# Optimization experiments

Hardware: AMD Instinct MI355X
Metric: run time of the kernel (lower is better)

The kernel has to match this reference:

```python
import jax, jax.numpy as jnp
import numpy as np

DIM = 512
D = 256
SCALE = D ** (-0.5)


def setup_inputs() -> dict:
    key = jax.random.key(0)
    ks = jax.random.split(key, 7)
    B, N, K = 16, 4096, 32
    g = 0.1 * (6.0 / (DIM + D)) ** 0.5  # xavier_uniform with gain=0.1
    return {
        "E_patches": jax.random.normal(ks[0], (B, N, DIM), jnp.float32),
        "T_b5": jax.random.normal(ks[1], (B, K, DIM), jnp.float32),
        "P_batch": jax.random.uniform(ks[2], (B, N), jnp.float32),
        "Wq": jax.random.uniform(ks[3], (D, DIM), jnp.float32, -g, g),
        "Wk": jax.random.uniform(ks[4], (D, DIM), jnp.float32, -g, g),
        "Wv": jax.random.uniform(ks[5], (D, DIM), jnp.float32, -g, g),
        "Wo": jax.random.uniform(ks[6], (DIM, D), jnp.float32, -g, g),
    }


def reference(E_patches, T_b5, P_batch, Wq, Wk, Wv, Wo):
    # Projections (torch Linear: x @ W.T)
    Q = jnp.einsum('bkm,dm->bkd', T_b5, Wq)       # [B,K,D]
    Kp = jnp.einsum('bnm,dm->bnd', E_patches, Wk)  # [B,N,D]
    V = jnp.einsum('bnm,dm->bnd', E_patches, Wv)   # [B,N,D]
    scores = jnp.einsum('bkd,bnd->bkn', Q, Kp) * SCALE
    logP = jnp.log(jnp.clip(P_batch, 0.1, 0.9))    # [B,N]
    scores = scores + logP[:, None, :]             # additive log-prior bias
    A = jax.nn.softmax(scores, axis=-1)            # [B,K,N]
    F_agg = jnp.einsum('bkn,bnd->bkd', A, V)
    F_agg = jnp.einsum('bkd,md->bkm', F_agg, Wo)   # [B,K,DIM]
    F_agg = F_agg / (jnp.linalg.norm(F_agg, axis=-1, keepdims=True) + 1e-8)
    return (F_agg, A)
```

## Files before the change

### kernel.cpp

```cpp
#include <hip/hip_runtime.h>

typedef __bf16 bf16x8 __attribute__((ext_vector_type(8)));
typedef __bf16 bf16x4 __attribute__((ext_vector_type(4)));
typedef float  f32x4  __attribute__((ext_vector_type(4)));

__device__ __forceinline__ void cp16(void* lds, const void* g) {
  __builtin_amdgcn_global_load_lds(
      (const __attribute__((address_space(1))) unsigned int*)g,
      (__attribute__((address_space(3))) unsigned int*)lds, 16, 0, 0);
}

#define VMCNT0  asm volatile("s_waitcnt vmcnt(0)" ::: "memory")
#define LGKM0   asm volatile("s_waitcnt lgkmcnt(0)" ::: "memory")
#define BARRAW  __builtin_amdgcn_s_barrier
#define MFMA    __builtin_amdgcn_mfma_f32_16x16x32_bf16


__global__ __launch_bounds__(256) void cvt_small(const float* __restrict__ Wq,
                                                 const float* __restrict__ Wk,
                                                 const float* __restrict__ Wv,
                                                 const float* __restrict__ Wo,
                                                 const float* __restrict__ T,
                                                 __bf16* __restrict__ Wqb,
                                                 __bf16* __restrict__ Tbf,
                                                 __bf16* __restrict__ WkT,
                                                 float* __restrict__ WvT,
                                                 float* __restrict__ WoT) {
  const int idx = blockIdx.x * 256 + threadIdx.x;
  if (idx < 32768) {
    const int o = idx * 4;
    f32x4 v = *(const f32x4*)(Wq + o);
    bf16x4 b;
    b[0] = (__bf16)v[0]; b[1] = (__bf16)v[1];
    b[2] = (__bf16)v[2]; b[3] = (__bf16)v[3];
    *(bf16x4*)(Wqb + o) = b;
  } else if (idx < 98304) {
    const int o = (idx - 32768) * 4;
    f32x4 v = *(const f32x4*)(T + o);
    bf16x4 b;
    b[0] = (__bf16)v[0]; b[1] = (__bf16)v[1];
    b[2] = (__bf16)v[2]; b[3] = (__bf16)v[3];
    *(bf16x4*)(Tbf + o) = b;
  } else if (idx < 106496) {
    const int t2 = idx - 98304;
    const int d0 = (t2 >> 7) * 4, m0 = (t2 & 127) * 4;
    f32x4 r0 = *(const f32x4*)(Wk + (size_t)(d0 + 0) * 512 + m0);
    f32x4 r1 = *(const f32x4*)(Wk + (size_t)(d0 + 1) * 512 + m0);
    f32x4 r2 = *(const f32x4*)(Wk + (size_t)(d0 + 2) * 512 + m0);
    f32x4 r3 = *(const f32x4*)(Wk + (size_t)(d0 + 3) * 512 + m0);
#pragma unroll
    for (int j = 0; j < 4; ++j) {
      bf16x4 o;
      o[0] = (__bf16)r0[j]; o[1] = (__bf16)r1[j];
      o[2] = (__bf16)r2[j]; o[3] = (__bf16)r3[j];
      *(bf16x4*)(WkT + (size_t)(m0 + j) * 256 + d0) = o;
    }
  } else if (idx < 114688) {
    const int t2 = idx - 106496;
    const int d0 = (t2 >> 7) * 4, m0 = (t2 & 127) * 4;
    f32x4 r0 = *(const f32x4*)(Wv + (size_t)(d0 + 0) * 512 + m0);
    f32x4 r1 = *(const f32x4*)(Wv + (size_t)(d0 + 1) * 512 + m0);
    f32x4 r2 = *(const f32x4*)(Wv + (size_t)(d0 + 2) * 512 + m0);
    f32x4 r3 = *(const f32x4*)(Wv + (size_t)(d0 + 3) * 512 + m0);
#pragma unroll
    for (int j = 0; j < 4; ++j) {
      f32x4 o;
      o[0] = r0[j]; o[1] = r1[j]; o[2] = r2[j]; o[3] = r3[j];
      *(f32x4*)(WvT + (size_t)(m0 + j) * 256 + d0) = o;
    }
  } else {
    const int t2 = idx - 114688;
    const int m0 = (t2 >> 6) * 4, d0 = (t2 & 63) * 4;
    f32x4 r0 = *(const f32x4*)(Wo + (size_t)(m0 + 0) * 256 + d0);
    f32x4 r1 = *(const f32x4*)(Wo + (size_t)(m0 + 1) * 256 + d0);
    f32x4 r2 = *(const f32x4*)(Wo + (size_t)(m0 + 2) * 256 + d0);
    f32x4 r3 = *(const f32x4*)(Wo + (size_t)(m0 + 3) * 256 + d0);
#pragma unroll
    for (int j = 0; j < 4; ++j) {
      f32x4 o;
      o[0] = r0[j]; o[1] = r1[j]; o[2] = r2[j]; o[3] = r3[j];
      *(f32x4*)(WoT + (size_t)(d0 + j) * 512 + m0) = o;
    }
  }
}

__global__ __launch_bounds__(256) void qproj(const __bf16* __restrict__ Wqb,
                                             const __bf16* __restrict__ Tbf,
                                             __bf16* __restrict__ Qw) {
  __shared__ __align__(16) __bf16 At[4096];
  __shared__ __align__(16) __bf16 Bt[4096];
  const int tid = threadIdx.x, lane = tid & 63;
  const int q = lane >> 4, ln = lane & 15;
  const int w = tid >> 6, wm = w >> 1, wn = w & 1;
  const int t = blockIdx.x;
  const int nbase = (t & 3) * 128;
  const int mbase = (t >> 2) * 128;
  f32x4 acc[4][4] = {};
  for (int kt = 0; kt < 16; ++kt) {
    const int k0 = kt * 32;
    __syncthreads();
#pragma unroll
    for (int s = 0; s < 2; ++s) {
      const int cbase = (tid & 192) + s * 256;
      const int cc = cbase + lane;
      const int row = cc >> 2, kc = (cc & 3) * 8;
      cp16(&At[cbase * 8], Wqb + (size_t)(mbase + row) * 512 + k0 + kc);
      cp16(&Bt[cbase * 8], Tbf + (size_t)(nbase + row) * 512 + k0 + kc);
    }
    __syncthreads();
    bf16x8 af[4], bfr[4];
#pragma unroll
    for (int f = 0; f < 4; ++f) {
      af[f]  = *(const bf16x8*)&At[(wm * 64 + f * 16 + ln) * 32 + q * 8];
      bfr[f] = *(const bf16x8*)&Bt[(wn * 64 + f * 16 + ln) * 32 + q * 8];
    }
#pragma unroll
    for (int fm = 0; fm < 4; ++fm)
#pragma unroll
      for (int fn = 0; fn < 4; ++fn)
        acc[fm][fn] = MFMA(af[fm], bfr[fn], acc[fm][fn], 0, 0, 0);
  }
#pragma unroll
  for (int fm = 0; fm < 4; ++fm)
#pragma unroll
    for (int fn = 0; fn < 4; ++fn) {
      const int m = mbase + wm * 64 + fm * 16 + q * 4;
      const int n = nbase + wn * 64 + fn * 16 + ln;
      f32x4 v = acc[fm][fn];
      bf16x4 o;
      o[0] = (__bf16)v[0]; o[1] = (__bf16)v[1];
      o[2] = (__bf16)v[2]; o[3] = (__bf16)v[3];
      *(bf16x4*)&Qw[(size_t)n * 256 + m] = o;
    }
}

__global__ __launch_bounds__(256) void qwk(const __bf16* __restrict__ WkT,
                                           const __bf16* __restrict__ Qwp,
                                           __bf16* __restrict__ QWkb) {
  __shared__ __align__(16) __bf16 At[4096];
  __shared__ __align__(16) __bf16 Bt[4096];
  const int tid = threadIdx.x, lane = tid & 63;
  const int q = lane >> 4, ln = lane & 15;
  const int w = tid >> 6, wm = w >> 1, wn = w & 1;
  const int t = blockIdx.x;
  const int nbase = (t & 3) * 128;
  const int mbase = (t >> 2) * 128;
  f32x4 acc[4][4] = {};
  for (int kt = 0; kt < 8; ++kt) {
    const int k0 = kt * 32;
    __syncthreads();
#pragma unroll
    for (int s = 0; s < 2; ++s) {
      const int cbase = (tid & 192) + s * 256;
      const int cc = cbase + lane;
      const int row = cc >> 2, kc = (cc & 3) * 8;
      cp16(&At[cbase * 8], WkT + (size_t)(mbase + row) * 256 + k0 + kc);
      cp16(&Bt[cbase * 8], Qwp + (size_t)(nbase + row) * 256 + k0 + kc);
    }
    __syncthreads();
    bf16x8 af[4], bfr[4];
#pragma unroll
    for (int f = 0; f < 4; ++f) {
      af[f]  = *(const bf16x8*)&At[(wm * 64 + f * 16 + ln) * 32 + q * 8];
      bfr[f] = *(const bf16x8*)&Bt[(wn * 64 + f * 16 + ln) * 32 + q * 8];
    }
#pragma unroll
    for (int fm = 0; fm < 4; ++fm)
#pragma unroll
      for (int fn = 0; fn < 4; ++fn)
        acc[fm][fn] = MFMA(af[fm], bfr[fn], acc[fm][fn], 0, 0, 0);
  }
#pragma unroll
  for (int fm = 0; fm < 4; ++fm)
#pragma unroll
    for (int fn = 0; fn < 4; ++fn) {
      const int m = mbase + wm * 64 + fm * 16 + q * 4;
      const int n = nbase + wn * 64 + fn * 16 + ln;
      f32x4 v = acc[fm][fn];
      bf16x4 o;
      o[0] = (__bf16)v[0]; o[1] = (__bf16)v[1];
      o[2] = (__bf16)v[2]; o[3] = (__bf16)v[3];
      *(bf16x4*)&QWkb[(size_t)n * 512 + m] = o;
    }
}

__device__ __forceinline__ void load_e(f32x4 (&ev)[16], const float* Eb,
                                       int s, int rg, int cg0) {
#pragma unroll
  for (int i = 0; i < 4; ++i) {
    const int cg = cg0 + i * 32;
#pragma unroll
    for (int r = 0; r < 4; ++r)
      ev[i * 4 + r] = *(const f32x4*)(Eb + (size_t)(s * 32 + rg * 4 + r) * 512 + cg * 4);
  }
}
__device__ __forceinline__ void cvtwrite_e(const f32x4 (&ev)[16], __bf16* Er,
                                           char* EtT, int rg, int cg0) {
#pragma unroll
  for (int i = 0; i < 4; ++i) {
    const int cg = cg0 + i * 32;
#pragma unroll
    for (int r = 0; r < 4; ++r) {
      bf16x4 rw;
      rw[0] = (__bf16)ev[i*4+r][0]; rw[1] = (__bf16)ev[i*4+r][1];
      rw[2] = (__bf16)ev[i*4+r][2]; rw[3] = (__bf16)ev[i*4+r][3];
      *(bf16x4*)((char*)Er + (size_t)(rg * 4 + r) * 1040 + cg * 8) = rw;
    }
#pragma unroll
    for (int j = 0; j < 4; ++j) {
      bf16x4 tw;
      tw[0] = (__bf16)ev[i*4+0][j]; tw[1] = (__bf16)ev[i*4+1][j];
      tw[2] = (__bf16)ev[i*4+2][j]; tw[3] = (__bf16)ev[i*4+3][j];
      const int m = cg * 4 + j;
      const int u = (rg >> 1) ^ (m & 3);
      *(bf16x4*)(EtT + (size_t)m * 80 + u * 16 + (rg & 1) * 8) = tw;
    }
  }
}
__device__ __forceinline__ void phase1(int s, const bf16x8 (&qf)[16],
                                       const __bf16* Er, __bf16* Plds,
                                       const float* Lp, float* rsum,
                                       int kf, int nf, int q, int ln) {
  f32x4 sacc = {0.f, 0.f, 0.f, 0.f};
#pragma unroll
  for (int kk = 0; kk < 16; ++kk) {
    bf16x8 bb = *(const bf16x8*)((char*)Er + (size_t)(nf * 16 + ln) * 1040 + kk * 64 + q * 16);
    sacc = MFMA(qf[kk], bb, sacc, 0, 0, 0);
  }
  const float lp = Lp[s * 32 + nf * 16 + ln];
  float pv[4];
#pragma unroll
  for (int r = 0; r < 4; ++r) {
    pv[r] = __expf(sacc[r] * 0.0625f + lp);
    *((__bf16*)((char*)Plds + (size_t)(kf * 16 + q * 4 + r) * 80) + nf * 16 + ln) = (__bf16)pv[r];
  }
#pragma unroll
  for (int mm = 1; mm < 16; mm <<= 1)
#pragma unroll
    for (int r = 0; r < 4; ++r) pv[r] += __shfl_xor(pv[r], mm, 64);
  if (ln == 0) {
#pragma unroll
    for (int r = 0; r < 4; ++r) atomicAdd(&rsum[kf * 16 + q * 4 + r], pv[r]);
  }
}
__device__ __forceinline__ void phase2(f32x4 (&facc)[2][8], const __bf16* Plds,
                                       const char* EtT, int w, int q, int ln,
                                       int tid, bf16x4* pr) {
  bf16x8 pa0 = *(const bf16x8*)((char*)Plds + (size_t)(ln) * 80 + q * 16);
  bf16x8 pa1 = *(const bf16x8*)((char*)Plds + (size_t)(16 + ln) * 80 + q * 16);
#pragma unroll
  for (int mf = 0; mf < 8; ++mf) {
    const int m = w * 128 + mf * 16 + ln;
    const int u = q ^ (m & 3);
    bf16x8 vb = *(const bf16x8*)(EtT + (size_t)m * 80 + u * 16);
    facc[0][mf] = MFMA(pa0, vb, facc[0][mf], 0, 0, 0);
    facc[1][mf] = MFMA(pa1, vb, facc[1][mf], 0, 0, 0);
  }
  *pr = *(const bf16x4*)((char*)Plds + (size_t)(tid >> 3) * 80 + (tid & 7) * 8);
}

__global__ __launch_bounds__(256, 2) void fused_main(
    const float* __restrict__ E, const __bf16* __restrict__ QWkb,
    const float* __restrict__ Pb, __bf16* __restrict__ Pws,
    float* __restrict__ Fpart, float* __restrict__ rowsum) {
  __shared__ __align__(16) __bf16 Er[32 * 520];
  __shared__ __align__(16) char  EtT[512 * 80];
  __shared__ __align__(16) __bf16 Plds[32 * 40];
  __shared__ __align__(16) float Lp[128];
  __shared__ float rsum[32];

  const int tid = threadIdx.x;
  const int lane = tid & 63;
  const int q = lane >> 4, ln = lane & 15;
  const int w = tid >> 6;
  const int kf = w >> 1;
  const int nf = w & 1;
  const int b = blockIdx.y, c = blockIdx.x;
  const int rg = tid >> 5;
  const int cg0 = tid & 31;

  const float* Eb = E + ((size_t)b * 4096 + (size_t)c * 128) * 512;

  bf16x8 qf[16];
  {
    const __bf16* qr = QWkb + (size_t)(b * 32 + kf * 16 + ln) * 512 + q * 8;
#pragma unroll
    for (int kk = 0; kk < 16; ++kk) qf[kk] = *(const bf16x8*)(qr + kk * 32);
  }
  if (tid < 128) {
    float p = Pb[b * 4096 + c * 128 + tid];
    Lp[tid] = __logf(fminf(fmaxf(p, 0.1f), 0.9f));
  }
  if (tid < 32) rsum[tid] = 0.f;

  f32x4 ev[16];
  load_e(ev, Eb, 0, rg, cg0);

  f32x4 facc[2][8] = {};
  bf16x4 pr0, pr1, pr2, pr3;

  VMCNT0;
  cvtwrite_e(ev, Er, EtT, rg, cg0);
  load_e(ev, Eb, 1, rg, cg0);
  LGKM0; BARRAW();
  phase1(0, qf, Er, Plds, Lp, rsum, kf, nf, q, ln);
  LGKM0; BARRAW();
  phase2(facc, Plds, EtT, w, q, ln, tid, &pr0);
  BARRAW();
  VMCNT0;
  cvtwrite_e(ev, Er, EtT, rg, cg0);
  load_e(ev, Eb, 2, rg, cg0);
  LGKM0; BARRAW();
  phase1(1, qf, Er, Plds, Lp, rsum, kf, nf, q, ln);
  LGKM0; BARRAW();
  phase2(facc, Plds, EtT, w, q, ln, tid, &pr1);
  BARRAW();
  VMCNT0;
  cvtwrite_e(ev, Er, EtT, rg, cg0);
  load_e(ev, Eb, 3, rg, cg0);
  LGKM0; BARRAW();
  phase1(2, qf, Er, Plds, Lp, rsum, kf, nf, q, ln);
  LGKM0; BARRAW();
  phase2(facc, Plds, EtT, w, q, ln, tid, &pr2);
  BARRAW();
  VMCNT0;
  cvtwrite_e(ev, Er, EtT, rg, cg0);
  LGKM0; BARRAW();
  phase1(3, qf, Er, Plds, Lp, rsum, kf, nf, q, ln);
  LGKM0; BARRAW();
  phase2(facc, Plds, EtT, w, q, ln, tid, &pr3);

  {
    const int prow = tid >> 3, pc = (tid & 7) * 4;
    __bf16* pwr = Pws + (size_t)(b * 32 + prow) * 4096 + c * 128 + pc;
    *(bf16x4*)(pwr)      = pr0;
    *(bf16x4*)(pwr + 32) = pr1;
    *(bf16x4*)(pwr + 64) = pr2;
    *(bf16x4*)(pwr + 96) = pr3;
  }
  float* Fp = Fpart + ((size_t)c * 512 + b * 32) * 512;
#pragma unroll
  for (int kf2 = 0; kf2 < 2; ++kf2)
#pragma unroll
    for (int mf = 0; mf < 8; ++mf)
#pragma unroll
      for (int r = 0; r < 4; ++r)
        Fp[(size_t)(kf2 * 16 + q * 4 + r) * 512 + w * 128 + mf * 16 + ln] = facc[kf2][mf][r];
  if (tid < 32) atomicAdd(&rowsum[b * 32 + tid], rsum[tid]);
}

__global__ __launch_bounds__(256) void norm_p(const __bf16* __restrict__ Pws,
                                              const float* __restrict__ rowsum,
                                              float* __restrict__ Aout) {
  const size_t idx = ((size_t)blockIdx.x * 256 + threadIdx.x) * 4;
  const int row = (int)(idx >> 12);
  const float invs = 1.0f / rowsum[row];
  bf16x4 p = *(const bf16x4*)(Pws + idx);
  f32x4 o;
  o[0] = (float)p[0] * invs; o[1] = (float)p[1] * invs;
  o[2] = (float)p[2] * invs; o[3] = (float)p[3] * invs;
  *(f32x4*)(Aout + idx) = o;
}

__global__ __launch_bounds__(256) void final_kernel(const float* __restrict__ Fpart,
                                                    const float* __restrict__ WvT,
                                                    const float* __restrict__ WoT,
                                                    float* __restrict__ Fout) {
  __shared__ float fl[512];
  __shared__ float agg[256];
  __shared__ float f2b[512];
  __shared__ float redbuf[4];
  const int row = blockIdx.x;
  const int t = threadIdx.x;
  const int lane = t & 63;
  const int w = t >> 6;

  {
    float s0 = 0.f, s1 = 0.f;
#pragma unroll
    for (int cc = 0; cc < 32; ++cc) {
      const float* p = Fpart + (size_t)cc * 262144 + (size_t)row * 512;
      s0 += p[t]; s1 += p[t + 256];
    }
    fl[t] = s0; fl[t + 256] = s1;
  }
  __syncthreads();

  {
    float a0 = 0.f, a1 = 0.f, a2 = 0.f, a3 = 0.f;
    for (int m = 0; m < 512; m += 4) {
      a0 += fl[m]     * WvT[(size_t)(m + 0) * 256 + t];
      a1 += fl[m + 1] * WvT[(size_t)(m + 1) * 256 + t];
      a2 += fl[m + 2] * WvT[(size_t)(m + 2) * 256 + t];
      a3 += fl[m + 3] * WvT[(size_t)(m + 3) * 256 + t];
    }
    agg[t] = (a0 + a1) + (a2 + a3);
  }
  __syncthreads();

  {
    float b0 = 0.f, b1 = 0.f, b2 = 0.f, b3 = 0.f;
    float c0 = 0.f, c1 = 0.f, c2 = 0.f, c3 = 0.f;
    for (int d = 0; d < 256; d += 4) {
      const float g0 = agg[d], g1 = agg[d + 1], g2 = agg[d + 2], g3 = agg[d + 3];
      b0 += g0 * WoT[(size_t)(d + 0) * 512 + t];
      b1 += g1 * WoT[(size_t)(d + 1) * 512 + t];
      b2 += g2 * WoT[(size_t)(d + 2) * 512 + t];
      b3 += g3 * WoT[(size_t)(d + 3) * 512 + t];
      c0 += g0 * WoT[(size_t)(d + 0) * 512 + t + 256];
      c1 += g1 * WoT[(size_t)(d + 1) * 512 + t + 256];
      c2 += g2 * WoT[(size_t)(d + 2) * 512 + t + 256];
      c3 += g3 * WoT[(size_t)(d + 3) * 512 + t + 256];
    }
    f2b[t] = (b0 + b1) + (b2 + b3);
    f2b[t + 256] = (c0 + c1) + (c2 + c3);
  }
  __syncthreads();

  {
    const float x0 = f2b[t], x1 = f2b[t + 256];
    float ps = x0 * x0 + x1 * x1;
#pragma unroll
    for (int mm = 1; mm < 64; mm <<= 1) ps += __shfl_xor(ps, mm, 64);
    if (lane == 0) redbuf[w] = ps;
  }
  __syncthreads();
  {
    const float tot = redbuf[0] + redbuf[1] + redbuf[2] + redbuf[3];
    const float sc = 1.0f / (sqrtf(tot) + 1e-8f);
    Fout[(size_t)row * 512 + t] = f2b[t] * sc;
    Fout[(size_t)row * 512 + t + 256] = f2b[t + 256] * sc;
  }
}

extern "C" void kernel_launch(void* const* d_in, const int* in_sizes, int n_in,
                              void* d_out, int out_size, void* d_ws, size_t ws_size,
                              hipStream_t stream) {
  const float* E  = (const float*)d_in[0];
  const float* T  = (const float*)d_in[1];
  const float* Pb = (const float*)d_in[2];
  const float* Wq = (const float*)d_in[3];
  const float* Wk = (const float*)d_in[4];
  const float* Wv = (const float*)d_in[5];
  const float* Wo = (const float*)d_in[6];

  float* out  = (float*)d_out;
  float* Fout = out;
  float* Aout = out + 262144;

  char* ws = (char*)d_ws;
  float*  Fpart = (float*)ws;
  __bf16* Pws   = (__bf16*)(ws + 33554432);
  __bf16* Tbf   = (__bf16*)(ws + 37748736);
  __bf16* Wqb   = (__bf16*)(ws + 38273024);
  __bf16* WkT   = (__bf16*)(ws + 38535168);
  float*  WvT   = (float*)(ws + 38797312);
  __bf16* Qw    = (__bf16*)(ws + 39321600);
  __bf16* QWkb  = (__bf16*)(ws + 39583744);
  float*  rowsum = (float*)(ws + 40108032);
  float*  WoT   = (float*)(ws + 40110080);

  hipMemsetAsync(rowsum, 0, 2048, stream);

  cvt_small<<<480, 256, 0, stream>>>(Wq, Wk, Wv, Wo, T, Wqb, Tbf, WkT, WvT, WoT);
  qproj<<<8, 256, 0, stream>>>(Wqb, Tbf, Qw);
  qwk<<<16, 256, 0, stream>>>(WkT, Qw, QWkb);
  fused_main<<<dim3(32, 16), 256, 0, stream>>>(E, QWkb, Pb, Pws, Fpart, rowsum);
  norm_p<<<2048, 256, 0, stream>>>(Pws, rowsum, Aout);
  final_kernel<<<512, 256, 0, stream>>>(Fpart, WvT, WoT, Fout);
}
```

Before: 268.2 us.

## Halve per-block N tile, read score operand from global, process two rows per final block

The main fused kernel now handles 64 patches per block instead of 128 and launches twice as many blocks. It drops the row-major bf16 LDS copy of E: phase1 reads E straight from global (cache-resident) and converts it in registers, which frees LDS and allows 3 blocks per CU. The cost is that the Fpart partial buffer doubles in size (64 chunks), so the final kernel sums more partials. To offset that, the final kernel handles two rows per block and reuses the Wv/Wo loads across both rows.

```diff
diff --git a/kernel.cpp b/kernel.cpp
--- a/kernel.cpp
+++ b/kernel.cpp
@@ -194,18 +194,11 @@
       ev[i * 4 + r] = *(const f32x4*)(Eb + (size_t)(s * 32 + rg * 4 + r) * 512 + cg * 4);
   }
 }
-__device__ __forceinline__ void cvtwrite_e(const f32x4 (&ev)[16], __bf16* Er,
-                                           char* EtT, int rg, int cg0) {
+__device__ __forceinline__ void cvtwrite_t(const f32x4 (&ev)[16], char* EtT,
+                                           int rg, int cg0) {
 #pragma unroll
   for (int i = 0; i < 4; ++i) {
     const int cg = cg0 + i * 32;
-#pragma unroll
-    for (int r = 0; r < 4; ++r) {
-      bf16x4 rw;
-      rw[0] = (__bf16)ev[i*4+r][0]; rw[1] = (__bf16)ev[i*4+r][1];
-      rw[2] = (__bf16)ev[i*4+r][2]; rw[3] = (__bf16)ev[i*4+r][3];
-      *(bf16x4*)((char*)Er + (size_t)(rg * 4 + r) * 1040 + cg * 8) = rw;
-    }
 #pragma unroll
     for (int j = 0; j < 4; ++j) {
       bf16x4 tw;
@@ -217,14 +210,21 @@
     }
   }
 }
-__device__ __forceinline__ void phase1(int s, const bf16x8 (&qf)[16],
-                                       const __bf16* Er, __bf16* Plds,
-                                       const float* Lp, float* rsum,
-                                       int kf, int nf, int q, int ln) {
+__device__ __forceinline__ void phase1g(int s, const bf16x8 (&qf)[16],
+                                        const float* Eb, __bf16* Plds,
+                                        const float* Lp, float* rsum,
+                                        int kf, int nf, int q, int ln) {
+  const float* er = Eb + (size_t)(s * 32 + nf * 16 + ln) * 512 + q * 8;
   f32x4 sacc = {0.f, 0.f, 0.f, 0.f};
 #pragma unroll
   for (int kk = 0; kk < 16; ++kk) {
-    bf16x8 bb = *(const bf16x8*)((char*)Er + (size_t)(nf * 16 + ln) * 1040 + kk * 64 + q * 16);
+    f32x4 e0 = *(const f32x4*)(er + kk * 32);
+    f32x4 e1 = *(const f32x4*)(er + kk * 32 + 4);
+    bf16x8 bb;
+    bb[0] = (__bf16)e0[0]; bb[1] = (__bf16)e0[1];
+    bb[2] = (__bf16)e0[2]; bb[3] = (__bf16)e0[3];
+    bb[4] = (__bf16)e1[0]; bb[5] = (__bf16)e1[1];
+    bb[6] = (__bf16)e1[2]; bb[7] = (__bf16)e1[3];
     sacc = MFMA(qf[kk], bb, sacc, 0, 0, 0);
   }
   const float lp = Lp[s * 32 + nf * 16 + ln];
@@ -259,14 +259,13 @@
   *pr = *(const bf16x4*)((char*)Plds + (size_t)(tid >> 3) * 80 + (tid & 7) * 8);
 }
 
-__global__ __launch_bounds__(256, 2) void fused_main(
+__global__ __launch_bounds__(256, 3) void fused_main(
     const float* __restrict__ E, const __bf16* __restrict__ QWkb,
     const float* __restrict__ Pb, __bf16* __restrict__ Pws,
     float* __restrict__ Fpart, float* __restrict__ rowsum) {
-  __shared__ __align__(16) __bf16 Er[32 * 520];
   __shared__ __align__(16) char  EtT[512 * 80];
   __shared__ __align__(16) __bf16 Plds[32 * 40];
-  __shared__ __align__(16) float Lp[128];
+  __shared__ __align__(16) float Lp[64];
   __shared__ float rsum[32];
 
   const int tid = threadIdx.x;
@@ -279,7 +278,7 @@
   const int rg = tid >> 5;
   const int cg0 = tid & 31;
 
-  const float* Eb = E + ((size_t)b * 4096 + (size_t)c * 128) * 512;
+  const float* Eb = E + ((size_t)b * 4096 + (size_t)c * 64) * 512;
 
   bf16x8 qf[16];
   {
@@ -287,8 +286,8 @@
 #pragma unroll
     for (int kk = 0; kk < 16; ++kk) qf[kk] = *(const bf16x8*)(qr + kk * 32);
   }
-  if (tid < 128) {
-    float p = Pb[b * 4096 + c * 128 + tid];
+  if (tid < 64) {
+    float p = Pb[b * 4096 + c * 64 + tid];
     Lp[tid] = __logf(fminf(fmaxf(p, 0.1f), 0.9f));
   }
   if (tid < 32) rsum[tid] = 0.f;
@@ -297,46 +296,28 @@
   load_e(ev, Eb, 0, rg, cg0);
 
   f32x4 facc[2][8] = {};
-  bf16x4 pr0, pr1, pr2, pr3;
+  bf16x4 pr0, pr1;
 
   VMCNT0;
-  cvtwrite_e(ev, Er, EtT, rg, cg0);
+  cvtwrite_t(ev, EtT, rg, cg0);
   load_e(ev, Eb, 1, rg, cg0);
   LGKM0; BARRAW();
-  phase1(0, qf, Er, Plds, Lp, rsum, kf, nf, q, ln);
+  phase1g(0, qf, Eb, Plds, Lp, rsum, kf, nf, q, ln);
   LGKM0; BARRAW();
   phase2(facc, Plds, EtT, w, q, ln, tid, &pr0);
   BARRAW();
   VMCNT0;
-  cvtwrite_e(ev, Er, EtT, rg, cg0);
-  load_e(ev, Eb, 2, rg, cg0);
+  cvtwrite_t(ev, EtT, rg, cg0);
   LGKM0; BARRAW();
-  phase1(1, qf, Er, Plds, Lp, rsum, kf, nf, q, ln);
+  phase1g(1, qf, Eb, Plds, Lp, rsum, kf, nf, q, ln);
   LGKM0; BARRAW();
   phase2(facc, Plds, EtT, w, q, ln, tid, &pr1);
-  BARRAW();
-  VMCNT0;
-  cvtwrite_e(ev, Er, EtT, rg, cg0);
-  load_e(ev, Eb, 3, rg, cg0);
-  LGKM0; BARRAW();
-  phase1(2, qf, Er, Plds, Lp, rsum, kf, nf, q, ln);
-  LGKM0; BARRAW();
-  phase2(facc, Plds, EtT, w, q, ln, tid, &pr2);
-  BARRAW();
-  VMCNT0;
-  cvtwrite_e(ev, Er, EtT, rg, cg0);
-  LGKM0; BARRAW();
-  phase1(3, qf, Er, Plds, Lp, rsum, kf, nf, q, ln);
-  LGKM0; BARRAW();
-  phase2(facc, Plds, EtT, w, q, ln, tid, &pr3);
 
   {
     const int prow = tid >> 3, pc = (tid & 7) * 4;
-    __bf16* pwr = Pws + (size_t)(b * 32 + prow) * 4096 + c * 128 + pc;
+    __bf16* pwr = Pws + (size_t)(b * 32 + prow) * 4096 + c * 64 + pc;
     *(bf16x4*)(pwr)      = pr0;
     *(bf16x4*)(pwr + 32) = pr1;
-    *(bf16x4*)(pwr + 64) = pr2;
-    *(bf16x4*)(pwr + 96) = pr3;
   }
   float* Fp = Fpart + ((size_t)c * 512 + b * 32) * 512;
 #pragma unroll
@@ -366,70 +347,80 @@
                                                     const float* __restrict__ WvT,
                                                     const float* __restrict__ WoT,
                                                     float* __restrict__ Fout) {
-  __shared__ float fl[512];
-  __shared__ float agg[256];
-  __shared__ float f2b[512];
-  __shared__ float redbuf[4];
-  const int row = blockIdx.x;
+  __shared__ float fl[2][512];
+  __shared__ float agg[2][256];
+  __shared__ float f2b[2][512];
+  __shared__ float redbuf[2][4];
+  const int r0 = blockIdx.x * 2;
   const int t = threadIdx.x;
   const int lane = t & 63;
   const int w = t >> 6;
 
+#pragma unroll
+  for (int r = 0; r < 2; ++r) {
+    float s0 = 0.f, s1 = 0.f;
+#pragma unroll
+    for (int cc = 0; cc < 64; ++cc) {
+      const float* p = Fpart + (size_t)cc * 262144 + (size_t)(r0 + r) * 512;
+      s0 += p[t]; s1 += p[t + 256];
+    }
+    fl[r][t] = s0; fl[r][t + 256] = s1;
+  }
+  __syncthreads();
+
   {
-    float s0 = 0.f, s1 = 0.f;
-#pragma unroll
-    for (int cc = 0; cc < 32; ++cc) {
-      const float* p = Fpart + (size_t)cc * 262144 + (size_t)row * 512;
-      s0 += p[t]; s1 += p[t + 256];
-    }
-    fl[t] = s0; fl[t + 256] = s1;
+    float a00 = 0.f, a01 = 0.f, a02 = 0.f, a03 = 0.f;
+    float a10 = 0.f, a11 = 0.f, a12 = 0.f, a13 = 0.f;
+    for (int m = 0; m < 512; m += 4) {
+      const float w0 = WvT[(size_t)(m + 0) * 256 + t];
+      const float w1 = WvT[(size_t)(m + 1) * 256 + t];
+      const float w2 = WvT[(size_t)(m + 2) * 256 + t];
+      const float w3 = WvT[(size_t)(m + 3) * 256 + t];
+      a00 += fl[0][m] * w0; a01 += fl[0][m + 1] * w1;
+      a02 += fl[0][m + 2] * w2; a03 += fl[0][m + 3] * w3;
+      a10 += fl[1][m] * w0; a11 += fl[1][m + 1] * w1;
+      a12 += fl[1][m + 2] * w2; a13 += fl[1][m + 3] * w3;
+    }
+    agg[0][t] = (a00 + a01) + (a02 + a03);
+    agg[1][t] = (a10 + a11) + (a12 + a13);
   }
   __syncthreads();
 
   {
-    float a0 = 0.f, a1 = 0.f, a2 = 0.f, a3 = 0.f;
-    for (int m = 0; m < 512; m += 4) {
-      a0 += fl[m]     * WvT[(size_t)(m + 0) * 256 + t];
-      a1 += fl[m + 1] * WvT[(size_t)(m + 1) * 256 + t];
-      a2 += fl[m + 2] * WvT[(size_t)(m + 2) * 256 + t];
-      a3 += fl[m + 3] * WvT[(size_t)(m + 3) * 256 + t];
-    }
-    agg[t] = (a0 + a1) + (a2 + a3);
+    float b0 = 0.f, b1 = 0.f, c0 = 0.f, c1 = 0.f;
+    float d0a = 0.f, d1a = 0.f, e0 = 0.f, e1 = 0.f;
+    for (int d = 0; d < 256; d += 2) {
+      const float g00 = agg[0][d], g01 = agg[0][d + 1];
+      const float g10 = agg[1][d], g11 = agg[1][d + 1];
+      const float w0 = WoT[(size_t)(d + 0) * 512 + t];
+      const float w1 = WoT[(size_t)(d + 1) * 512 + t];
+      const float x0 = WoT[(size_t)(d + 0) * 512 + t + 256];
+      const float x1 = WoT[(size_t)(d + 1) * 512 + t + 256];
+      b0 += g00 * w0; b1 += g01 * w1;
+      c0 += g00 * x0; c1 += g01 * x1;
+      d0a += g10 * w0; d1a += g11 * w1;
+      e0 += g10 * x0; e1 += g11 * x1;
+    }
+    f2b[0][t] = b0 + b1;       f2b[0][t + 256] = c0 + c1;
+    f2b[1][t] = d0a + d1a;     f2b[1][t + 256] = e0 + e1;
   }
   __syncthreads();
 
-  {
-    float b0 = 0.f, b1 = 0.f, b2 = 0.f, b3 = 0.f;
-    float c0 = 0.f, c1 = 0.f, c2 = 0.f, c3 = 0.f;
-    for (int d = 0; d < 256; d += 4) {
-      const float g0 = agg[d], g1 = agg[d + 1], g2 = agg[d + 2], g3 = agg[d + 3];
-      b0 += g0 * WoT[(size_t)(d + 0) * 512 + t];
-      b1 += g1 * WoT[(size_t)(d + 1) * 512 + t];
-      b2 += g2 * WoT[(size_t)(d + 2) * 512 + t];
-      b3 += g3 * WoT[(size_t)(d + 3) * 512 + t];
-      c0 += g0 * WoT[(size_t)(d + 0) * 512 + t + 256];
-      c1 += g1 * WoT[(size_t)(d + 1) * 512 + t + 256];
-      c2 += g2 * WoT[(size_t)(d + 2) * 512 + t + 256];
-      c3 += g3 * WoT[(size_t)(d + 3) * 512 + t + 256];
-    }
-    f2b[t] = (b0 + b1) + (b2 + b3);
-    f2b[t + 256] = (c0 + c1) + (c2 + c3);
+#pragma unroll
+  for (int r = 0; r < 2; ++r) {
+    const float x0 = f2b[r][t], x1 = f2b[r][t + 256];
+    float ps = x0 * x0 + x1 * x1;
+#pragma unroll
+    for (int mm = 1; mm < 64; mm <<= 1) ps += __shfl_xor(ps, mm, 64);
+    if (lane == 0) redbuf[r][w] = ps;
   }
   __syncthreads();
-
-  {
-    const float x0 = f2b[t], x1 = f2b[t + 256];
-    float ps = x0 * x0 + x1 * x1;
-#pragma unroll
-    for (int mm = 1; mm < 64; mm <<= 1) ps += __shfl_xor(ps, mm, 64);
-    if (lane == 0) redbuf[w] = ps;
-  }
-  __syncthreads();
-  {
-    const float tot = redbuf[0] + redbuf[1] + redbuf[2] + redbuf[3];
+#pragma unroll
+  for (int r = 0; r < 2; ++r) {
+    const float tot = redbuf[r][0] + redbuf[r][1] + redbuf[r][2] + redbuf[r][3];
     const float sc = 1.0f / (sqrtf(tot) + 1e-8f);
-    Fout[(size_t)row * 512 + t] = f2b[t] * sc;
-    Fout[(size_t)row * 512 + t + 256] = f2b[t + 256] * sc;
+    Fout[(size_t)(r0 + r) * 512 + t] = f2b[r][t] * sc;
+    Fout[(size_t)(r0 + r) * 512 + t + 256] = f2b[r][t + 256] * sc;
   }
 }
 
@@ -450,22 +441,22 @@
 
   char* ws = (char*)d_ws;
   float*  Fpart = (float*)ws;
-  __bf16* Pws   = (__bf16*)(ws + 33554432);
-  __bf16* Tbf   = (__bf16*)(ws + 37748736);
-  __bf16* Wqb   = (__bf16*)(ws + 38273024);
-  __bf16* WkT   = (__bf16*)(ws + 38535168);
-  float*  WvT   = (float*)(ws + 38797312);
-  __bf16* Qw    = (__bf16*)(ws + 39321600);
-  __bf16* QWkb  = (__bf16*)(ws + 39583744);
-  float*  rowsum = (float*)(ws + 40108032);
-  float*  WoT   = (float*)(ws + 40110080);
+  __bf16* Pws   = (__bf16*)(ws + 67108864);
+  __bf16* Tbf   = (__bf16*)(ws + 71303168);
+  __bf16* Wqb   = (__bf16*)(ws + 71827456);
+  __bf16* WkT   = (__bf16*)(ws + 72089600);
+  float*  WvT   = (float*)(ws + 72351744);
+  __bf16* Qw    = (__bf16*)(ws + 72876032);
+  __bf16* QWkb  = (__bf16*)(ws + 73138176);
+  float*  rowsum = (float*)(ws + 73662464);
+  float*  WoT   = (float*)(ws + 73664512);
 
   hipMemsetAsync(rowsum, 0, 2048, stream);
 
   cvt_small<<<480, 256, 0, stream>>>(Wq, Wk, Wv, Wo, T, Wqb, Tbf, WkT, WvT, WoT);
   qproj<<<8, 256, 0, stream>>>(Wqb, Tbf, Qw);
   qwk<<<16, 256, 0, stream>>>(WkT, Qw, QWkb);
-  fused_main<<<dim3(32, 16), 256, 0, stream>>>(E, QWkb, Pb, Pws, Fpart, rowsum);
+  fused_main<<<dim3(64, 16), 256, 0, stream>>>(E, QWkb, Pb, Pws, Fpart, rowsum);
   norm_p<<<2048, 256, 0, stream>>>(Pws, rowsum, Aout);
-  final_kernel<<<512, 256, 0, stream>>>(Fpart, WvT, WoT, Fout);
-}
+  final_kernel<<<256, 256, 0, stream>>>(Fpart, WvT, WoT, Fout);
+}
```

After: 356.4 us. 1.33x slower.

## Double fused_main block to 512 threads with split-K score reduction

Applied to the files above, without the earlier changes.

Raises the fused attention kernel's block from 256 to 512 threads (8 waves). Each thread now loads half as much of E per stage, and the phase-2 output columns are split across more waves. The QK score MFMA is split along K between two wave halves and combined through a new LDS reduction buffer. This is meant to add in-flight memory loads and MFMA parallelism per CU, at the cost of an extra barrier per stage and more LDS use, which may limit co-resident blocks.

```diff
diff --git a/kernel.cpp b/kernel.cpp
--- a/kernel.cpp
+++ b/kernel.cpp
@@ -184,27 +184,27 @@
     }
 }
 
-__device__ __forceinline__ void load_e(f32x4 (&ev)[16], const float* Eb,
-                                       int s, int rg, int cg0) {
-#pragma unroll
-  for (int i = 0; i < 4; ++i) {
-    const int cg = cg0 + i * 32;
+__device__ __forceinline__ void load_e6(f32x4 (&ev)[8], const float* Eb,
+                                        int s, int rg, int cg0) {
+#pragma unroll
+  for (int i = 0; i < 2; ++i) {
+    const int cg = cg0 + i * 64;
 #pragma unroll
     for (int r = 0; r < 4; ++r)
       ev[i * 4 + r] = *(const f32x4*)(Eb + (size_t)(s * 32 + rg * 4 + r) * 512 + cg * 4);
   }
 }
-__device__ __forceinline__ void cvtwrite_e(const f32x4 (&ev)[16], __bf16* Er,
-                                           char* EtT, int rg, int cg0) {
-#pragma unroll
-  for (int i = 0; i < 4; ++i) {
-    const int cg = cg0 + i * 32;
+__device__ __forceinline__ void cvtwrite6(const f32x4 (&ev)[8], char* Er,
+                                          char* EtT, int rg, int cg0) {
+#pragma unroll
+  for (int i = 0; i < 2; ++i) {
+    const int cg = cg0 + i * 64;
 #pragma unroll
     for (int r = 0; r < 4; ++r) {
       bf16x4 rw;
       rw[0] = (__bf16)ev[i*4+r][0]; rw[1] = (__bf16)ev[i*4+r][1];
       rw[2] = (__bf16)ev[i*4+r][2]; rw[3] = (__bf16)ev[i*4+r][3];
-      *(bf16x4*)((char*)Er + (size_t)(rg * 4 + r) * 1040 + cg * 8) = rw;
+      *(bf16x4*)(Er + (size_t)(rg * 4 + r) * 1040 + cg * 8) = rw;
     }
 #pragma unroll
     for (int j = 0; j < 4; ++j) {
@@ -217,75 +217,36 @@
     }
   }
 }
-__device__ __forceinline__ void phase1(int s, const bf16x8 (&qf)[16],
-                                       const __bf16* Er, __bf16* Plds,
-                                       const float* Lp, float* rsum,
-                                       int kf, int nf, int q, int ln) {
-  f32x4 sacc = {0.f, 0.f, 0.f, 0.f};
-#pragma unroll
-  for (int kk = 0; kk < 16; ++kk) {
-    bf16x8 bb = *(const bf16x8*)((char*)Er + (size_t)(nf * 16 + ln) * 1040 + kk * 64 + q * 16);
-    sacc = MFMA(qf[kk], bb, sacc, 0, 0, 0);
-  }
-  const float lp = Lp[s * 32 + nf * 16 + ln];
-  float pv[4];
-#pragma unroll
-  for (int r = 0; r < 4; ++r) {
-    pv[r] = __expf(sacc[r] * 0.0625f + lp);
-    *((__bf16*)((char*)Plds + (size_t)(kf * 16 + q * 4 + r) * 80) + nf * 16 + ln) = (__bf16)pv[r];
-  }
-#pragma unroll
-  for (int mm = 1; mm < 16; mm <<= 1)
-#pragma unroll
-    for (int r = 0; r < 4; ++r) pv[r] += __shfl_xor(pv[r], mm, 64);
-  if (ln == 0) {
-#pragma unroll
-    for (int r = 0; r < 4; ++r) atomicAdd(&rsum[kf * 16 + q * 4 + r], pv[r]);
-  }
-}
-__device__ __forceinline__ void phase2(f32x4 (&facc)[2][8], const __bf16* Plds,
-                                       const char* EtT, int w, int q, int ln,
-                                       int tid, bf16x4* pr) {
-  bf16x8 pa0 = *(const bf16x8*)((char*)Plds + (size_t)(ln) * 80 + q * 16);
-  bf16x8 pa1 = *(const bf16x8*)((char*)Plds + (size_t)(16 + ln) * 80 + q * 16);
-#pragma unroll
-  for (int mf = 0; mf < 8; ++mf) {
-    const int m = w * 128 + mf * 16 + ln;
-    const int u = q ^ (m & 3);
-    bf16x8 vb = *(const bf16x8*)(EtT + (size_t)m * 80 + u * 16);
-    facc[0][mf] = MFMA(pa0, vb, facc[0][mf], 0, 0, 0);
-    facc[1][mf] = MFMA(pa1, vb, facc[1][mf], 0, 0, 0);
-  }
-  *pr = *(const bf16x4*)((char*)Plds + (size_t)(tid >> 3) * 80 + (tid & 7) * 8);
-}
-
-__global__ __launch_bounds__(256, 2) void fused_main(
+
+__global__ __launch_bounds__(512, 4) void fused_main(
     const float* __restrict__ E, const __bf16* __restrict__ QWkb,
     const float* __restrict__ Pb, __bf16* __restrict__ Pws,
     float* __restrict__ Fpart, float* __restrict__ rowsum) {
-  __shared__ __align__(16) __bf16 Er[32 * 520];
-  __shared__ __align__(16) char  EtT[512 * 80];
-  __shared__ __align__(16) __bf16 Plds[32 * 40];
-  __shared__ __align__(16) float Lp[128];
+  __shared__ __align__(16) char Er[32 * 1040];
+  __shared__ __align__(16) char EtT[512 * 80];
+  __shared__ __align__(16) char Plds[32 * 80];
+  __shared__ __align__(16) float Sred[32 * 32];
+  __shared__ float Lp[128];
   __shared__ float rsum[32];
 
   const int tid = threadIdx.x;
   const int lane = tid & 63;
   const int q = lane >> 4, ln = lane & 15;
   const int w = tid >> 6;
-  const int kf = w >> 1;
+  const int kf = (w >> 1) & 1;
   const int nf = w & 1;
+  const int kh = w >> 2;
   const int b = blockIdx.y, c = blockIdx.x;
-  const int rg = tid >> 5;
-  const int cg0 = tid & 31;
+  const int rg = tid >> 6;
+  const int cg0 = tid & 63;
 
   const float* Eb = E + ((size_t)b * 4096 + (size_t)c * 128) * 512;
 
-  bf16x8 qf[16];
-  {
-    const __bf16* qr = QWkb + (size_t)(b * 32 + kf * 16 + ln) * 512 + q * 8;
-#pragma unroll
-    for (int kk = 0; kk < 16; ++kk) qf[kk] = *(const bf16x8*)(qr + kk * 32);
+  bf16x8 qf[8];
+  {
+    const __bf16* qr = QWkb + (size_t)(b * 32 + kf * 16 + ln) * 512 + kh * 256 + q * 8;
+#pragma unroll
+    for (int kkl = 0; kkl < 8; ++kkl) qf[kkl] = *(const bf16x8*)(qr + kkl * 32);
   }
   if (tid < 128) {
     float p = Pb[b * 4096 + c * 128 + tid];
@@ -293,59 +254,79 @@
   }
   if (tid < 32) rsum[tid] = 0.f;
 
-  f32x4 ev[16];
-  load_e(ev, Eb, 0, rg, cg0);
-
-  f32x4 facc[2][8] = {};
-  bf16x4 pr0, pr1, pr2, pr3;
-
-  VMCNT0;
-  cvtwrite_e(ev, Er, EtT, rg, cg0);
-  load_e(ev, Eb, 1, rg, cg0);
-  LGKM0; BARRAW();
-  phase1(0, qf, Er, Plds, Lp, rsum, kf, nf, q, ln);
-  LGKM0; BARRAW();
-  phase2(facc, Plds, EtT, w, q, ln, tid, &pr0);
-  BARRAW();
-  VMCNT0;
-  cvtwrite_e(ev, Er, EtT, rg, cg0);
-  load_e(ev, Eb, 2, rg, cg0);
-  LGKM0; BARRAW();
-  phase1(1, qf, Er, Plds, Lp, rsum, kf, nf, q, ln);
-  LGKM0; BARRAW();
-  phase2(facc, Plds, EtT, w, q, ln, tid, &pr1);
-  BARRAW();
-  VMCNT0;
-  cvtwrite_e(ev, Er, EtT, rg, cg0);
-  load_e(ev, Eb, 3, rg, cg0);
-  LGKM0; BARRAW();
-  phase1(2, qf, Er, Plds, Lp, rsum, kf, nf, q, ln);
-  LGKM0; BARRAW();
-  phase2(facc, Plds, EtT, w, q, ln, tid, &pr2);
-  BARRAW();
-  VMCNT0;
-  cvtwrite_e(ev, Er, EtT, rg, cg0);
-  LGKM0; BARRAW();
-  phase1(3, qf, Er, Plds, Lp, rsum, kf, nf, q, ln);
-  LGKM0; BARRAW();
-  phase2(facc, Plds, EtT, w, q, ln, tid, &pr3);
-
-  {
-    const int prow = tid >> 3, pc = (tid & 7) * 4;
-    __bf16* pwr = Pws + (size_t)(b * 32 + prow) * 4096 + c * 128 + pc;
-    *(bf16x4*)(pwr)      = pr0;
-    *(bf16x4*)(pwr + 32) = pr1;
-    *(bf16x4*)(pwr + 64) = pr2;
-    *(bf16x4*)(pwr + 96) = pr3;
-  }
+  f32x4 ev[8];
+  load_e6(ev, Eb, 0, rg, cg0);
+  f32x4 facc[2][4] = {};
+
+#pragma unroll
+  for (int s = 0; s < 4; ++s) {
+    VMCNT0;
+    cvtwrite6(ev, Er, EtT, rg, cg0);
+    if (s < 3) load_e6(ev, Eb, s + 1, rg, cg0);
+    LGKM0; BARRAW();
+
+    {
+      f32x4 sacc = {0.f, 0.f, 0.f, 0.f};
+#pragma unroll
+      for (int kkl = 0; kkl < 8; ++kkl) {
+        const int kk = kh * 8 + kkl;
+        bf16x8 bb = *(const bf16x8*)(Er + (size_t)(nf * 16 + ln) * 1040 + kk * 64 + q * 16);
+        sacc = MFMA(qf[kkl], bb, sacc, 0, 0, 0);
+      }
+      if (kh) {
+#pragma unroll
+        for (int r = 0; r < 4; ++r)
+          Sred[(kf * 16 + q * 4 + r) * 32 + nf * 16 + ln] = sacc[r];
+      }
+      LGKM0; BARRAW();
+      if (!kh) {
+        const float lp = Lp[s * 32 + nf * 16 + ln];
+        float pv[4];
+#pragma unroll
+        for (int r = 0; r < 4; ++r) {
+          const float sv = sacc[r] + Sred[(kf * 16 + q * 4 + r) * 32 + nf * 16 + ln];
+          pv[r] = __expf(sv * 0.0625f + lp);
+          *((__bf16*)(Plds + (size_t)(kf * 16 + q * 4 + r) * 80) + nf * 16 + ln) = (__bf16)pv[r];
+        }
+#pragma unroll
+        for (int mm = 1; mm < 16; mm <<= 1)
+#pragma unroll
+          for (int r = 0; r < 4; ++r) pv[r] += __shfl_xor(pv[r], mm, 64);
+        if (ln == 0) {
+#pragma unroll
+          for (int r = 0; r < 4; ++r) atomicAdd(&rsum[kf * 16 + q * 4 + r], pv[r]);
+        }
+      }
+      LGKM0; BARRAW();
+    }
+
+    {
+      bf16x8 pa0 = *(const bf16x8*)(Plds + (size_t)(ln) * 80 + q * 16);
+      bf16x8 pa1 = *(const bf16x8*)(Plds + (size_t)(16 + ln) * 80 + q * 16);
+#pragma unroll
+      for (int mf = 0; mf < 4; ++mf) {
+        const int m = w * 64 + mf * 16 + ln;
+        const int u = q ^ (m & 3);
+        bf16x8 vb = *(const bf16x8*)(EtT + (size_t)m * 80 + u * 16);
+        facc[0][mf] = MFMA(pa0, vb, facc[0][mf], 0, 0, 0);
+        facc[1][mf] = MFMA(pa1, vb, facc[1][mf], 0, 0, 0);
+      }
+    }
+    if (tid < 256) {
+      bf16x4 pc4 = *(const bf16x4*)(Plds + (size_t)(tid >> 3) * 80 + (tid & 7) * 8);
+      *(bf16x4*)(Pws + (size_t)(b * 32 + (tid >> 3)) * 4096 + c * 128 + s * 32 + (tid & 7) * 4) = pc4;
+    }
+    if (s < 3) BARRAW();
+  }
+
   float* Fp = Fpart + ((size_t)c * 512 + b * 32) * 512;
 #pragma unroll
   for (int kf2 = 0; kf2 < 2; ++kf2)
 #pragma unroll
-    for (int mf = 0; mf < 8; ++mf)
+    for (int mf = 0; mf < 4; ++mf)
 #pragma unroll
       for (int r = 0; r < 4; ++r)
-        Fp[(size_t)(kf2 * 16 + q * 4 + r) * 512 + w * 128 + mf * 16 + ln] = facc[kf2][mf][r];
+        Fp[(size_t)(kf2 * 16 + q * 4 + r) * 512 + w * 64 + mf * 16 + ln] = facc[kf2][mf][r];
   if (tid < 32) atomicAdd(&rowsum[b * 32 + tid], rsum[tid]);
 }
 
@@ -465,7 +446,7 @@
   cvt_small<<<480, 256, 0, stream>>>(Wq, Wk, Wv, Wo, T, Wqb, Tbf, WkT, WvT, WoT);
   qproj<<<8, 256, 0, stream>>>(Wqb, Tbf, Qw);
   qwk<<<16, 256, 0, stream>>>(WkT, Qw, QWkb);
-  fused_main<<<dim3(32, 16), 256, 0, stream>>>(E, QWkb, Pb, Pws, Fpart, rowsum);
+  fused_main<<<dim3(32, 16), 512, 0, stream>>>(E, QWkb, Pb, Pws, Fpart, rowsum);
   norm_p<<<2048, 256, 0, stream>>>(Pws, rowsum, Aout);
   final_kernel<<<512, 256, 0, stream>>>(Fpart, WvT, WoT, Fout);
 }
```

Measured after the change: 277.0 us. +3.3%, slower.
